# Optimization experiments

Measured on AMD Instinct MI355X. Metric: run time of the kernel, lower is better.

Reference implementation:

```python
import jax, jax.numpy as jnp
import numpy as np

DIM = 512
INNER = 512        # heads(8) * dim_head(64)
OUT_DIM = 256
SCALE = 64 ** -0.5  # dim_head ** -0.5
BN_EPS = 1e-5


def setup_inputs() -> dict:
    key = jax.random.key(0)
    ks = jax.random.split(key, 8)
    B, H, W = 2, 96, 320
    return {
        "left_feat": jax.random.normal(ks[0], (B, DIM, H, W), jnp.float32),
        "right_feat": jax.random.normal(ks[1], (B, DIM, H, W), jnp.float32),
        "wq": jax.random.normal(ks[2], (INNER, DIM), jnp.float32) * (DIM ** -0.5),
        "wk": jax.random.normal(ks[3], (INNER, DIM), jnp.float32) * (DIM ** -0.5),
        "wv": jax.random.normal(ks[4], (INNER, DIM), jnp.float32) * (DIM ** -0.5),
        "w1": jax.random.normal(ks[5], (OUT_DIM, INNER * 2), jnp.float32) * ((INNER * 2) ** -0.5),
        "bn_gamma": jnp.ones((OUT_DIM,), jnp.float32),
        "bn_beta": jnp.zeros((OUT_DIM,), jnp.float32),
        "bn_mean": jnp.zeros((OUT_DIM,), jnp.float32),
        "bn_var": jnp.ones((OUT_DIM,), jnp.float32),
        "w2": jax.random.normal(ks[6], (OUT_DIM, OUT_DIM), jnp.float32) * (OUT_DIM ** -0.5),
    }


def reference(left_feat, right_feat, wq, wk, wv, w1, bn_gamma, bn_beta, bn_mean, bn_var, w2):
    # conv1x1 projections, directly producing channels-last [b, h, w, c]
    q = jnp.einsum('bchw,oc->bhwo', left_feat, wq)
    k = jnp.einsum('bchw,oc->bhwo', right_feat, wk)
    v = jnp.einsum('bchw,oc->bhwo', right_feat, wv)
    # cross-attention along width, independently per (batch, row)
    dots = jnp.einsum('bhwc,bhxc->bhwx', q, k) * SCALE   # [b, h, w, w]
    attn = jax.nn.softmax(dots, axis=-1)
    out = jnp.einsum('bhwx,bhxc->bhwc', attn, v)         # [b, h, w, c]
    out = out.transpose(0, 3, 1, 2)                      # [b, c, h, w]
    new_left = jnp.concatenate([left_feat, out], axis=1)  # [b, 2*inner, h, w]
    # to_out: conv1x1 -> BN (eval mode, running stats) -> LeakyReLU(0.2) -> conv1x1
    y = jnp.einsum('bchw,oc->bohw', new_left, w1)
    inv = jax.lax.rsqrt(bn_var + BN_EPS)
    y = (y - bn_mean[None, :, None, None]) * (inv * bn_gamma)[None, :, None, None] \
        + bn_beta[None, :, None, None]
    y = jnp.where(y >= 0, y, 0.2 * y)
    return jnp.einsum('bchw,oc->bohw', y, w2)
```

## Files before the change

kernel.cpp:

```cpp
#include <hip/hip_runtime.h>

typedef __bf16 bf16x8 __attribute__((ext_vector_type(8)));
typedef float f32x4 __attribute__((ext_vector_type(4)));

#define MFMA16(a, b, c) __builtin_amdgcn_mfma_f32_16x16x32_bf16((a), (b), (c), 0, 0, 0)
#define GLOAD_LDS(gp, lp) __builtin_amdgcn_global_load_lds( \
    (const __attribute__((address_space(1))) void*)(uintptr_t)(const void*)(gp), \
    (__attribute__((address_space(3))) void*)(uintptr_t)(void*)(lp), 16, 0, 0)

#define NB 2
#define NC 512
#define NH 96
#define NW 320
#define PH 30720
#define NPIX 61440
#define NOUT 256

__device__ __forceinline__ unsigned short f2bf(float f) {
    union { float f; unsigned u; } v; v.f = f;
    unsigned r = v.u + 0x7fffu + ((v.u >> 16) & 1u);
    return (unsigned short)(r >> 16);
}

__global__ void k_cast(const float* __restrict__ src, unsigned short* __restrict__ dst, int n) {
    int i = blockIdx.x * 256 + threadIdx.x;
    if (i < n) dst[i] = f2bf(src[i]);
}

__global__ __launch_bounds__(256) void k_transpose(
        const float* __restrict__ L, const float* __restrict__ R,
        unsigned short* __restrict__ Lcl, unsigned short* __restrict__ Rcl) {
    __shared__ float t[64][65];
    int z = blockIdx.z;
    int b = z & 1, which = z >> 1;
    const float* src = which ? R : L;
    unsigned short* dst = which ? Rcl : Lcl;
    int c0 = blockIdx.y * 64;
    int p0 = blockIdx.x * 64;
    int tx = threadIdx.x & 63, ty = threadIdx.x >> 6;
#pragma unroll
    for (int i = 0; i < 16; ++i) {
        int cl = ty + i * 4;
        t[cl][tx] = src[(b * NC + c0 + cl) * PH + p0 + tx];
    }
    __syncthreads();
#pragma unroll
    for (int i = 0; i < 16; ++i) {
        int pl = ty + i * 4;
        dst[(b * PH + p0 + pl) * NC + c0 + tx] = f2bf(t[tx][pl]);
    }
}

template <int MODE>
__global__ __launch_bounds__(256) void k_gemm(
        const unsigned short* __restrict__ A0,
        const unsigned short* __restrict__ A1,
        const unsigned short* __restrict__ Bb,
        unsigned short* __restrict__ Dbf,
        float* __restrict__ Df32,
        const float* __restrict__ g, const float* __restrict__ be,
        const float* __restrict__ mu, const float* __restrict__ va) {
    constexpr int SA = (MODE == 4) ? NOUT : NC;
    constexpr int SB = (MODE == 3) ? 1024 : (MODE == 4) ? NOUT : NC;
    constexpr int KS = (MODE == 3) ? 32 : (MODE == 4) ? 8 : 16;
    constexpr int NTO = (MODE <= 2) ? 4 : 2;
    constexpr int TOT = 480 * NTO;

    __shared__ unsigned short Asm[128 * 32];
    __shared__ unsigned short Bsm[128 * 32];

    int pphys = blockIdx.x;
    int lgc = (pphys & 7) * (TOT / 8) + (pphys >> 3);
    int pixt = lgc / NTO, ot = lgc % NTO;
    const int mbase = ((MODE == 2 || MODE == 4) ? ot : pixt) * 128;
    const int nbase = ((MODE == 2 || MODE == 4) ? pixt : ot) * 128;

    const int lane = threadIdx.x & 63, w = threadIdx.x >> 6;
    const int lr = lane & 15, lg = lane >> 4;
    const int wr = w >> 1, wc = w & 1;

    auto stage = [&](unsigned short* lds, const unsigned short* src, int rowBase, int colOff) {
#pragma unroll
        for (int j = 0; j < 2; ++j) {
            int cb = w * 128 + j * 64;
            int c = cb + lane;
            int rstride = (lds == Asm) ? SA : SB;
            const unsigned short* gp = src + (size_t)(rowBase + (c >> 2)) * rstride + colOff + (c & 3) * 8;
            GLOAD_LDS(gp, lds + cb * 8);
        }
    };

    f32x4 acc[4][4] = {};

    for (int kc = 0; kc < KS; ++kc) {
        if constexpr (MODE == 3) {
            if (kc < 16) stage(Asm, A0, mbase, kc * 32);
            else         stage(Asm, A1, mbase, (kc - 16) * 32);
        } else {
            stage(Asm, A0, mbase, kc * 32);
        }
        stage(Bsm, Bb, nbase, kc * 32);
        __syncthreads();

        bf16x8 af[4], bfr[4];
#pragma unroll
        for (int i = 0; i < 4; ++i)
            af[i] = *reinterpret_cast<const bf16x8*>(Asm + (wr * 64 + i * 16 + lr) * 32 + lg * 8);
#pragma unroll
        for (int j = 0; j < 4; ++j)
            bfr[j] = *reinterpret_cast<const bf16x8*>(Bsm + (wc * 64 + j * 16 + lr) * 32 + lg * 8);
#pragma unroll
        for (int i = 0; i < 4; ++i)
#pragma unroll
            for (int j = 0; j < 4; ++j)
                acc[i][j] = MFMA16(af[i], bfr[j], acc[i][j]);
        __syncthreads();
    }

    const int lr4 = lg * 4;
    if constexpr (MODE <= 1) {
#pragma unroll
        for (int i = 0; i < 4; ++i)
#pragma unroll
            for (int j = 0; j < 4; ++j) {
                int ocol = nbase + wc * 64 + j * 16 + lr;
#pragma unroll
                for (int r = 0; r < 4; ++r) {
                    int prow = mbase + wr * 64 + i * 16 + lr4 + r;
                    Dbf[(size_t)prow * NC + ocol] = f2bf(acc[i][j][r]);
                }
            }
    } else if constexpr (MODE == 2) {
#pragma unroll
        for (int i = 0; i < 4; ++i)
#pragma unroll
            for (int j = 0; j < 4; ++j) {
                int pix = nbase + wc * 64 + j * 16 + lr;
                int b = pix / PH, ph = pix % PH;
                int hh = ph / NW, x = ph % NW;
#pragma unroll
                for (int r = 0; r < 4; ++r) {
                    int crow = mbase + wr * 64 + i * 16 + lr4 + r;
                    Dbf[((size_t)(b * NH + hh) * NC + crow) * NW + x] = f2bf(acc[i][j][r]);
                }
            }
    } else if constexpr (MODE == 3) {
#pragma unroll
        for (int j = 0; j < 4; ++j) {
            int o = nbase + wc * 64 + j * 16 + lr;
            float sc = g[o] * rsqrtf(va[o] + 1e-5f);
            float sh = be[o] - mu[o] * sc;
#pragma unroll
            for (int i = 0; i < 4; ++i)
#pragma unroll
                for (int r = 0; r < 4; ++r) {
                    int prow = mbase + wr * 64 + i * 16 + lr4 + r;
                    float y = acc[i][j][r] * sc + sh;
                    y = (y >= 0.f) ? y : 0.2f * y;
                    Dbf[(size_t)prow * NOUT + o] = f2bf(y);
                }
        }
    } else {
#pragma unroll
        for (int j = 0; j < 4; ++j) {
            int pix = nbase + wc * 64 + j * 16 + lr;
            int b = pix / PH, ph = pix % PH;
#pragma unroll
            for (int i = 0; i < 4; ++i)
#pragma unroll
                for (int r = 0; r < 4; ++r) {
                    int o = mbase + wr * 64 + i * 16 + lr4 + r;
                    Df32[((size_t)b * NOUT + o) * PH + ph] = acc[i][j][r];
                }
        }
    }
}

__global__ __launch_bounds__(256, 2) void k_attn(
        const unsigned short* __restrict__ Q, const unsigned short* __restrict__ K,
        const unsigned short* __restrict__ Vt, unsigned short* __restrict__ O) {
    __shared__ unsigned short P[64][328];
    __shared__ unsigned short KV[32 * 512];

    int pphys = blockIdx.x;
    int l = (pphys & 7) * 120 + (pphys >> 3);
    int head = l / 5, qt = l % 5;
    int b = head / NH, hh = head % NH;
    int lane = threadIdx.x & 63, w = threadIdx.x >> 6;
    int lr = lane & 15, lg = lane >> 4;
    int rowbase = b * PH + hh * NW;
    int qrow = rowbase + qt * 64 + w * 16 + lr;

    bf16x8 qf[16];
#pragma unroll
    for (int kc = 0; kc < 16; ++kc)
        qf[kc] = *reinterpret_cast<const bf16x8*>(Q + (size_t)qrow * NC + kc * 32 + lg * 8);

    f32x4 acc[20];
#pragma unroll
    for (int xt = 0; xt < 20; ++xt) acc[xt] = f32x4{0.f, 0.f, 0.f, 0.f};

#pragma unroll
    for (int s = 0; s < 10; ++s) {
#pragma unroll
        for (int j = 0; j < 8; ++j) {
            int r = w * 8 + j;
            const unsigned short* gp = K + (size_t)(rowbase + s * 32 + r) * NC + ((lane ^ (r & 7)) * 8);
            GLOAD_LDS(gp, KV + r * 512);
        }
        __syncthreads();
#pragma unroll
        for (int x2 = 0; x2 < 2; ++x2) {
            int rrow = x2 * 16 + lr;
            int rsw = lr & 7;
#pragma unroll
            for (int kc = 0; kc < 16; ++kc) {
                bf16x8 kf = *reinterpret_cast<const bf16x8*>(KV + rrow * 512 + (((kc * 4 + lg) ^ rsw) * 8));
                acc[s * 2 + x2] = MFMA16(qf[kc], kf, acc[s * 2 + x2]);
            }
        }
        __syncthreads();
    }

#pragma unroll
    for (int xt = 0; xt < 20; ++xt)
#pragma unroll
        for (int r = 0; r < 4; ++r) acc[xt][r] *= 0.125f;
    float m[4] = {-1e30f, -1e30f, -1e30f, -1e30f};
#pragma unroll
    for (int xt = 0; xt < 20; ++xt)
#pragma unroll
        for (int r = 0; r < 4; ++r) m[r] = fmaxf(m[r], acc[xt][r]);
#pragma unroll
    for (int mask = 1; mask < 16; mask <<= 1)
#pragma unroll
        for (int r = 0; r < 4; ++r) m[r] = fmaxf(m[r], __shfl_xor(m[r], mask));
    float s4[4] = {0.f, 0.f, 0.f, 0.f};
#pragma unroll
    for (int xt = 0; xt < 20; ++xt)
#pragma unroll
        for (int r = 0; r < 4; ++r) {
            float e = __expf(acc[xt][r] - m[r]);
            acc[xt][r] = e;
            s4[r] += e;
        }
#pragma unroll
    for (int mask = 1; mask < 16; mask <<= 1)
#pragma unroll
        for (int r = 0; r < 4; ++r) s4[r] += __shfl_xor(s4[r], mask);
#pragma unroll
    for (int xt = 0; xt < 20; ++xt)
#pragma unroll
        for (int r = 0; r < 4; ++r)
            P[w * 16 + lg * 4 + r][xt * 16 + lr] = f2bf(acc[xt][r]);
    __syncthreads();

    f32x4 oacc[32];
#pragma unroll
    for (int ct = 0; ct < 32; ++ct) oacc[ct] = f32x4{0.f, 0.f, 0.f, 0.f};

    int vbase = (b * NH + hh) * NC;
    for (int s = 0; s < 10; ++s) {
#pragma unroll
        for (int j = 0; j < 8; ++j) {
            int c = (w * 8 + j) * 16 + (lane >> 2);
            int qg = (lane & 3) ^ ((lane >> 3) & 3);
            const unsigned short* gp = Vt + (size_t)(vbase + c) * NW + s * 32 + qg * 8;
            GLOAD_LDS(gp, KV + (w * 8 + j) * 512);
        }
        __syncthreads();
        bf16x8 pf = *reinterpret_cast<const bf16x8*>(&P[w * 16 + lr][s * 32 + lg * 8]);
#pragma unroll
        for (int ct = 0; ct < 32; ++ct) {
            bf16x8 vf = *reinterpret_cast<const bf16x8*>(KV + ct * 512 + lr * 32 + ((lg ^ ((lr >> 1) & 3)) * 8));
            oacc[ct] = MFMA16(pf, vf, oacc[ct]);
        }
        __syncthreads();
    }

#pragma unroll
    for (int ct = 0; ct < 32; ++ct)
#pragma unroll
        for (int r = 0; r < 4; ++r) {
            int prow = rowbase + qt * 64 + w * 16 + lg * 4 + r;
            O[(size_t)prow * NC + ct * 16 + lr] = f2bf(oacc[ct][r] / s4[r]);
        }
}

extern "C" void kernel_launch(void* const* d_in, const int* in_sizes, int n_in,
                              void* d_out, int out_size, void* d_ws, size_t ws_size,
                              hipStream_t stream) {
    const float* left  = (const float*)d_in[0];
    const float* right = (const float*)d_in[1];
    const float* wq = (const float*)d_in[2];
    const float* wk = (const float*)d_in[3];
    const float* wv = (const float*)d_in[4];
    const float* w1 = (const float*)d_in[5];
    const float* bn_g = (const float*)d_in[6];
    const float* bn_b = (const float*)d_in[7];
    const float* bn_m = (const float*)d_in[8];
    const float* bn_v = (const float*)d_in[9];
    const float* w2 = (const float*)d_in[10];
    float* out = (float*)d_out;

    size_t off = 0;
    auto alloc = [&](size_t bytes) -> void* {
        void* p = (char*)d_ws + off;
        off += (bytes + 255) & ~(size_t)255;
        return p;
    };
    const size_t clb = (size_t)NPIX * NC * 2;
    unsigned short* Lcl = (unsigned short*)alloc(clb);
    unsigned short* Rcl = (unsigned short*)alloc(clb);
    unsigned short* Qb  = (unsigned short*)alloc(clb);
    unsigned short* Kb  = (unsigned short*)alloc(clb);
    unsigned short* Vt  = (unsigned short*)alloc(clb);
    unsigned short* Wqb = (unsigned short*)alloc((size_t)NC * NC * 2);
    unsigned short* Wkb = (unsigned short*)alloc((size_t)NC * NC * 2);
    unsigned short* Wvb = (unsigned short*)alloc((size_t)NC * NC * 2);
    unsigned short* W1b = (unsigned short*)alloc((size_t)NOUT * 1024 * 2);
    unsigned short* W2b = (unsigned short*)alloc((size_t)NOUT * NOUT * 2);
    unsigned short* AO = Rcl;
    unsigned short* Yb = Qb;

    k_cast<<<dim3((NC * NC + 255) / 256), 256, 0, stream>>>(wq, Wqb, NC * NC);
    k_cast<<<dim3((NC * NC + 255) / 256), 256, 0, stream>>>(wk, Wkb, NC * NC);
    k_cast<<<dim3((NC * NC + 255) / 256), 256, 0, stream>>>(wv, Wvb, NC * NC);
    k_cast<<<dim3((NOUT * 1024 + 255) / 256), 256, 0, stream>>>(w1, W1b, NOUT * 1024);
    k_cast<<<dim3((NOUT * NOUT + 255) / 256), 256, 0, stream>>>(w2, W2b, NOUT * NOUT);

    k_transpose<<<dim3(PH / 64, NC / 64, 4), 256, 0, stream>>>(left, right, Lcl, Rcl);

    k_gemm<0><<<dim3(1920), 256, 0, stream>>>(Lcl, nullptr, Wqb, Qb, nullptr, nullptr, nullptr, nullptr, nullptr);
    k_gemm<1><<<dim3(1920), 256, 0, stream>>>(Rcl, nullptr, Wkb, Kb, nullptr, nullptr, nullptr, nullptr, nullptr);
    k_gemm<2><<<dim3(1920), 256, 0, stream>>>(Wvb, nullptr, Rcl, Vt, nullptr, nullptr, nullptr, nullptr, nullptr);

    k_attn<<<dim3(960), 256, 0, stream>>>(Qb, Kb, Vt, AO);

    k_gemm<3><<<dim3(960), 256, 0, stream>>>(Lcl, AO, W1b, Yb, nullptr, bn_g, bn_b, bn_m, bn_v);

    k_gemm<4><<<dim3(960), 256, 0, stream>>>(W2b, nullptr, Yb, nullptr, out, nullptr, nullptr, nullptr, nullptr);
}
```

Measured before the change: 429.4 us.

## Fuse K/V projections into one kernel and register-prefetch K/V tiles in attention

Replaces the separate K and V projection GEMMs with a single kernel that loads each right-feature tile once and computes both K and the transposed V, so the shared input is read from memory only once. In the attention kernel, the direct global-to-LDS loads are replaced by register prefetch of the next K or V tile into a double-buffered LDS region, with setprio around the MFMA blocks, so loads can overlap compute. The cost is more registers and an extra barrier per step, which may lower occupancy.

```diff
diff --git a/kernel.cpp b/kernel.cpp
--- a/kernel.cpp
+++ b/kernel.cpp
@@ -2,6 +2,7 @@
 
 typedef __bf16 bf16x8 __attribute__((ext_vector_type(8)));
 typedef float f32x4 __attribute__((ext_vector_type(4)));
+typedef unsigned short u16x8 __attribute__((ext_vector_type(8)));
 
 #define MFMA16(a, b, c) __builtin_amdgcn_mfma_f32_16x16x32_bf16((a), (b), (c), 0, 0, 0)
 #define GLOAD_LDS(gp, lp) __builtin_amdgcn_global_load_lds( \
@@ -130,20 +131,6 @@
                     Dbf[(size_t)prow * NC + ocol] = f2bf(acc[i][j][r]);
                 }
             }
-    } else if constexpr (MODE == 2) {
-#pragma unroll
-        for (int i = 0; i < 4; ++i)
-#pragma unroll
-            for (int j = 0; j < 4; ++j) {
-                int pix = nbase + wc * 64 + j * 16 + lr;
-                int b = pix / PH, ph = pix % PH;
-                int hh = ph / NW, x = ph % NW;
-#pragma unroll
-                for (int r = 0; r < 4; ++r) {
-                    int crow = mbase + wr * 64 + i * 16 + lr4 + r;
-                    Dbf[((size_t)(b * NH + hh) * NC + crow) * NW + x] = f2bf(acc[i][j][r]);
-                }
-            }
     } else if constexpr (MODE == 3) {
 #pragma unroll
         for (int j = 0; j < 4; ++j) {
@@ -174,6 +161,93 @@
                 }
         }
     }
+}
+
+__global__ __launch_bounds__(256) void k_projkv(
+        const unsigned short* __restrict__ Rcl,
+        const unsigned short* __restrict__ Wk, const unsigned short* __restrict__ Wv,
+        unsigned short* __restrict__ Kb, unsigned short* __restrict__ Vt) {
+    __shared__ unsigned short Rsm[128 * 32];
+    __shared__ unsigned short Ksm[128 * 32];
+    __shared__ unsigned short Vsm[128 * 32];
+
+    int pphys = blockIdx.x;
+    int lgc = (pphys & 7) * 240 + (pphys >> 3);
+    int pixt = lgc / 4, j4 = lgc % 4;
+    const int pbase = pixt * 128;
+    const int obase = j4 * 128;
+
+    const int lane = threadIdx.x & 63, w = threadIdx.x >> 6;
+    const int lr = lane & 15, lg = lane >> 4;
+    const int wr = w >> 1, wc = w & 1;
+
+    auto stage = [&](unsigned short* lds, const unsigned short* src, int rowBase, int colOff) {
+#pragma unroll
+        for (int j = 0; j < 2; ++j) {
+            int cb = w * 128 + j * 64;
+            int c = cb + lane;
+            const unsigned short* gp = src + (size_t)(rowBase + (c >> 2)) * NC + colOff + (c & 3) * 8;
+            GLOAD_LDS(gp, lds + cb * 8);
+        }
+    };
+
+    f32x4 ak[4][4] = {};
+    f32x4 av[4][4] = {};
+
+    for (int kc = 0; kc < 16; ++kc) {
+        stage(Rsm, Rcl, pbase, kc * 32);
+        stage(Ksm, Wk, obase, kc * 32);
+        stage(Vsm, Wv, obase, kc * 32);
+        __syncthreads();
+
+        bf16x8 ra[4], rb[4], kb[4], va[4];
+#pragma unroll
+        for (int i = 0; i < 4; ++i) {
+            ra[i] = *reinterpret_cast<const bf16x8*>(Rsm + (wr * 64 + i * 16 + lr) * 32 + lg * 8);
+            va[i] = *reinterpret_cast<const bf16x8*>(Vsm + (wr * 64 + i * 16 + lr) * 32 + lg * 8);
+        }
+#pragma unroll
+        for (int j = 0; j < 4; ++j) {
+            rb[j] = *reinterpret_cast<const bf16x8*>(Rsm + (wc * 64 + j * 16 + lr) * 32 + lg * 8);
+            kb[j] = *reinterpret_cast<const bf16x8*>(Ksm + (wc * 64 + j * 16 + lr) * 32 + lg * 8);
+        }
+        __builtin_amdgcn_s_setprio(1);
+#pragma unroll
+        for (int i = 0; i < 4; ++i)
+#pragma unroll
+            for (int j = 0; j < 4; ++j) {
+                ak[i][j] = MFMA16(ra[i], kb[j], ak[i][j]);
+                av[i][j] = MFMA16(va[i], rb[j], av[i][j]);
+            }
+        __builtin_amdgcn_s_setprio(0);
+        __syncthreads();
+    }
+
+    const int lr4 = lg * 4;
+#pragma unroll
+    for (int i = 0; i < 4; ++i)
+#pragma unroll
+        for (int j = 0; j < 4; ++j) {
+            int ocol = obase + wc * 64 + j * 16 + lr;
+#pragma unroll
+            for (int r = 0; r < 4; ++r) {
+                int prow = pbase + wr * 64 + i * 16 + lr4 + r;
+                Kb[(size_t)prow * NC + ocol] = f2bf(ak[i][j][r]);
+            }
+        }
+#pragma unroll
+    for (int i = 0; i < 4; ++i)
+#pragma unroll
+        for (int j = 0; j < 4; ++j) {
+            int pix = pbase + wc * 64 + j * 16 + lr;
+            int b = pix / PH, ph = pix % PH;
+            int hh = ph / NW, x = ph % NW;
+#pragma unroll
+            for (int r = 0; r < 4; ++r) {
+                int crow = obase + wr * 64 + i * 16 + lr4 + r;
+                Vt[((size_t)(b * NH + hh) * NC + crow) * NW + x] = f2bf(av[i][j][r]);
+            }
+        }
 }
 
 __global__ __launch_bounds__(256, 2) void k_attn(
@@ -200,27 +274,61 @@
 #pragma unroll
     for (int xt = 0; xt < 20; ++xt) acc[xt] = f32x4{0.f, 0.f, 0.f, 0.f};
 
-#pragma unroll
-    for (int s = 0; s < 10; ++s) {
+    u16x8 kreg[4];
+    auto kload = [&](int t) {
+#pragma unroll
+        for (int j = 0; j < 4; ++j) {
+            int r = w * 4 + j;
+            kreg[j] = *reinterpret_cast<const u16x8*>(
+                K + (size_t)(rowbase + t * 16 + r) * NC + ((lane ^ (r & 7)) * 8));
+        }
+    };
+    auto kwrite = [&](int buf) {
+#pragma unroll
+        for (int j = 0; j < 4; ++j) {
+            int r = w * 4 + j;
+            *reinterpret_cast<u16x8*>(KV + (buf * 16 + r) * 512 + lane * 8) = kreg[j];
+        }
+    };
+
+    kload(0);
+    kwrite(0);
+    __syncthreads();
+#pragma unroll
+    for (int t = 0; t < 20; ++t) {
+        if (t + 1 < 20) kload(t + 1);
+        int buf = t & 1;
+        int rsw = lr & 7;
+        __builtin_amdgcn_s_setprio(1);
+#pragma unroll
+        for (int kc = 0; kc < 16; ++kc) {
+            bf16x8 kf = *reinterpret_cast<const bf16x8*>(
+                KV + (buf * 16 + lr) * 512 + (((kc * 4 + lg) ^ rsw) * 8));
+            acc[t] = MFMA16(qf[kc], kf, acc[t]);
+        }
+        __builtin_amdgcn_s_setprio(0);
+        __syncthreads();
+        if (t + 1 < 20) kwrite(buf ^ 1);
+        __syncthreads();
+    }
+
+    int vbase = (b * NH + hh) * NC;
+    u16x8 vreg[8];
+    auto vload = [&](int s) {
 #pragma unroll
         for (int j = 0; j < 8; ++j) {
-            int r = w * 8 + j;
-            const unsigned short* gp = K + (size_t)(rowbase + s * 32 + r) * NC + ((lane ^ (r & 7)) * 8);
-            GLOAD_LDS(gp, KV + r * 512);
-        }
-        __syncthreads();
-#pragma unroll
-        for (int x2 = 0; x2 < 2; ++x2) {
-            int rrow = x2 * 16 + lr;
-            int rsw = lr & 7;
-#pragma unroll
-            for (int kc = 0; kc < 16; ++kc) {
-                bf16x8 kf = *reinterpret_cast<const bf16x8*>(KV + rrow * 512 + (((kc * 4 + lg) ^ rsw) * 8));
-                acc[s * 2 + x2] = MFMA16(qf[kc], kf, acc[s * 2 + x2]);
-            }
-        }
-        __syncthreads();
-    }
+            int c = (w * 8 + j) * 16 + (lane >> 2);
+            int qg = (lane & 3) ^ ((lane >> 3) & 3);
+            vreg[j] = *reinterpret_cast<const u16x8*>(
+                Vt + (size_t)(vbase + c) * NW + s * 32 + qg * 8);
+        }
+    };
+    auto vwrite = [&]() {
+#pragma unroll
+        for (int j = 0; j < 8; ++j)
+            *reinterpret_cast<u16x8*>(KV + (w * 8 + j) * 512 + lane * 8) = vreg[j];
+    };
+    vload(0);
 
 #pragma unroll
     for (int xt = 0; xt < 20; ++xt)
@@ -254,27 +362,27 @@
         for (int r = 0; r < 4; ++r)
             P[w * 16 + lg * 4 + r][xt * 16 + lr] = f2bf(acc[xt][r]);
     __syncthreads();
+    vwrite();
+    __syncthreads();
 
     f32x4 oacc[32];
 #pragma unroll
     for (int ct = 0; ct < 32; ++ct) oacc[ct] = f32x4{0.f, 0.f, 0.f, 0.f};
 
-    int vbase = (b * NH + hh) * NC;
+#pragma unroll
     for (int s = 0; s < 10; ++s) {
-#pragma unroll
-        for (int j = 0; j < 8; ++j) {
-            int c = (w * 8 + j) * 16 + (lane >> 2);
-            int qg = (lane & 3) ^ ((lane >> 3) & 3);
-            const unsigned short* gp = Vt + (size_t)(vbase + c) * NW + s * 32 + qg * 8;
-            GLOAD_LDS(gp, KV + (w * 8 + j) * 512);
-        }
-        __syncthreads();
+        if (s + 1 < 10) vload(s + 1);
         bf16x8 pf = *reinterpret_cast<const bf16x8*>(&P[w * 16 + lr][s * 32 + lg * 8]);
+        __builtin_amdgcn_s_setprio(1);
 #pragma unroll
         for (int ct = 0; ct < 32; ++ct) {
-            bf16x8 vf = *reinterpret_cast<const bf16x8*>(KV + ct * 512 + lr * 32 + ((lg ^ ((lr >> 1) & 3)) * 8));
+            bf16x8 vf = *reinterpret_cast<const bf16x8*>(
+                KV + ct * 512 + lr * 32 + ((lg ^ ((lr >> 1) & 3)) * 8));
             oacc[ct] = MFMA16(pf, vf, oacc[ct]);
         }
+        __builtin_amdgcn_s_setprio(0);
+        __syncthreads();
+        if (s + 1 < 10) vwrite();
         __syncthreads();
     }
 
@@ -332,8 +440,7 @@
     k_transpose<<<dim3(PH / 64, NC / 64, 4), 256, 0, stream>>>(left, right, Lcl, Rcl);
 
     k_gemm<0><<<dim3(1920), 256, 0, stream>>>(Lcl, nullptr, Wqb, Qb, nullptr, nullptr, nullptr, nullptr, nullptr);
-    k_gemm<1><<<dim3(1920), 256, 0, stream>>>(Rcl, nullptr, Wkb, Kb, nullptr, nullptr, nullptr, nullptr, nullptr);
-    k_gemm<2><<<dim3(1920), 256, 0, stream>>>(Wvb, nullptr, Rcl, Vt, nullptr, nullptr, nullptr, nullptr, nullptr);
+    k_projkv<<<dim3(1920), 256, 0, stream>>>(Rcl, Wkb, Wvb, Kb, Vt);
 
     k_attn<<<dim3(960), 256, 0, stream>>>(Qb, Kb, Vt, AO);
 
```

Result: slower. 507.2 us (+18.1%).

## Double-buffer GEMM LDS tiles and prefetch attention K/V through registers

Applied to the files above, without the earlier changes.

The GEMM kernel now uses two LDS buffers per operand, so the next K-slice is issued before the MFMAs on the current one, with one barrier per iteration instead of two. The attention kernel replaces the direct global-to-LDS K and V loads with register prefetch: the next tile is loaded into registers while MFMAs run on the current LDS tile, then written to LDS. The K tile shrinks to 16 rows in a double buffer, and the first V tile is prefetched during the softmax. s_setprio raises wave priority around the MFMA blocks. The changes aim to hide global-load latency, but they double GEMM LDS use and add register pressure in the already register-heavy attention kernel, which could lower occupancy.

```diff
diff --git a/kernel.cpp b/kernel.cpp
--- a/kernel.cpp
+++ b/kernel.cpp
@@ -2,6 +2,7 @@
 
 typedef __bf16 bf16x8 __attribute__((ext_vector_type(8)));
 typedef float f32x4 __attribute__((ext_vector_type(4)));
+typedef unsigned short u16x8 __attribute__((ext_vector_type(8)));
 
 #define MFMA16(a, b, c) __builtin_amdgcn_mfma_f32_16x16x32_bf16((a), (b), (c), 0, 0, 0)
 #define GLOAD_LDS(gp, lp) __builtin_amdgcn_global_load_lds( \
@@ -66,8 +67,8 @@
     constexpr int NTO = (MODE <= 2) ? 4 : 2;
     constexpr int TOT = 480 * NTO;
 
-    __shared__ unsigned short Asm[128 * 32];
-    __shared__ unsigned short Bsm[128 * 32];
+    __shared__ unsigned short Asm[2][128 * 32];
+    __shared__ unsigned short Bsm[2][128 * 32];
 
     int pphys = blockIdx.x;
     int lgc = (pphys & 7) * (TOT / 8) + (pphys >> 3);
@@ -79,41 +80,56 @@
     const int lr = lane & 15, lg = lane >> 4;
     const int wr = w >> 1, wc = w & 1;
 
-    auto stage = [&](unsigned short* lds, const unsigned short* src, int rowBase, int colOff) {
+    auto stageA = [&](int buf, int kc) {
+        const unsigned short* srcA = A0;
+        int colOff = kc * 32;
+        if constexpr (MODE == 3) {
+            if (kc >= 16) { srcA = A1; colOff = (kc - 16) * 32; }
+        }
 #pragma unroll
         for (int j = 0; j < 2; ++j) {
             int cb = w * 128 + j * 64;
             int c = cb + lane;
-            int rstride = (lds == Asm) ? SA : SB;
-            const unsigned short* gp = src + (size_t)(rowBase + (c >> 2)) * rstride + colOff + (c & 3) * 8;
-            GLOAD_LDS(gp, lds + cb * 8);
+            const unsigned short* gp = srcA + (size_t)(mbase + (c >> 2)) * SA + colOff + (c & 3) * 8;
+            GLOAD_LDS(gp, Asm[buf] + cb * 8);
+        }
+    };
+    auto stageB = [&](int buf, int kc) {
+#pragma unroll
+        for (int j = 0; j < 2; ++j) {
+            int cb = w * 128 + j * 64;
+            int c = cb + lane;
+            const unsigned short* gp = Bb + (size_t)(nbase + (c >> 2)) * SB + kc * 32 + (c & 3) * 8;
+            GLOAD_LDS(gp, Bsm[buf] + cb * 8);
         }
     };
 
     f32x4 acc[4][4] = {};
 
+    stageA(0, 0);
+    stageB(0, 0);
+    __syncthreads();
+
     for (int kc = 0; kc < KS; ++kc) {
-        if constexpr (MODE == 3) {
-            if (kc < 16) stage(Asm, A0, mbase, kc * 32);
-            else         stage(Asm, A1, mbase, (kc - 16) * 32);
-        } else {
-            stage(Asm, A0, mbase, kc * 32);
-        }
-        stage(Bsm, Bb, nbase, kc * 32);
-        __syncthreads();
-
+        int cur = kc & 1;
+        if (kc + 1 < KS) {
+            stageA(cur ^ 1, kc + 1);
+            stageB(cur ^ 1, kc + 1);
+        }
         bf16x8 af[4], bfr[4];
 #pragma unroll
         for (int i = 0; i < 4; ++i)
-            af[i] = *reinterpret_cast<const bf16x8*>(Asm + (wr * 64 + i * 16 + lr) * 32 + lg * 8);
+            af[i] = *reinterpret_cast<const bf16x8*>(Asm[cur] + (wr * 64 + i * 16 + lr) * 32 + lg * 8);
 #pragma unroll
         for (int j = 0; j < 4; ++j)
-            bfr[j] = *reinterpret_cast<const bf16x8*>(Bsm + (wc * 64 + j * 16 + lr) * 32 + lg * 8);
+            bfr[j] = *reinterpret_cast<const bf16x8*>(Bsm[cur] + (wc * 64 + j * 16 + lr) * 32 + lg * 8);
+        __builtin_amdgcn_s_setprio(1);
 #pragma unroll
         for (int i = 0; i < 4; ++i)
 #pragma unroll
             for (int j = 0; j < 4; ++j)
                 acc[i][j] = MFMA16(af[i], bfr[j], acc[i][j]);
+        __builtin_amdgcn_s_setprio(0);
         __syncthreads();
     }
 
@@ -200,27 +216,61 @@
 #pragma unroll
     for (int xt = 0; xt < 20; ++xt) acc[xt] = f32x4{0.f, 0.f, 0.f, 0.f};
 
-#pragma unroll
-    for (int s = 0; s < 10; ++s) {
+    u16x8 kreg[4];
+    auto kload = [&](int t) {
+#pragma unroll
+        for (int j = 0; j < 4; ++j) {
+            int r = w * 4 + j;
+            kreg[j] = *reinterpret_cast<const u16x8*>(
+                K + (size_t)(rowbase + t * 16 + r) * NC + ((lane ^ (r & 7)) * 8));
+        }
+    };
+    auto kwrite = [&](int buf) {
+#pragma unroll
+        for (int j = 0; j < 4; ++j) {
+            int r = w * 4 + j;
+            *reinterpret_cast<u16x8*>(KV + (buf * 16 + r) * 512 + lane * 8) = kreg[j];
+        }
+    };
+
+    kload(0);
+    kwrite(0);
+    __syncthreads();
+#pragma unroll
+    for (int t = 0; t < 20; ++t) {
+        if (t + 1 < 20) kload(t + 1);
+        int buf = t & 1;
+        int rsw = lr & 7;
+        __builtin_amdgcn_s_setprio(1);
+#pragma unroll
+        for (int kc = 0; kc < 16; ++kc) {
+            bf16x8 kf = *reinterpret_cast<const bf16x8*>(
+                KV + (buf * 16 + lr) * 512 + (((kc * 4 + lg) ^ rsw) * 8));
+            acc[t] = MFMA16(qf[kc], kf, acc[t]);
+        }
+        __builtin_amdgcn_s_setprio(0);
+        __syncthreads();
+        if (t + 1 < 20) kwrite(buf ^ 1);
+        __syncthreads();
+    }
+
+    int vbase = (b * NH + hh) * NC;
+    u16x8 vreg[8];
+    auto vload = [&](int s) {
 #pragma unroll
         for (int j = 0; j < 8; ++j) {
-            int r = w * 8 + j;
-            const unsigned short* gp = K + (size_t)(rowbase + s * 32 + r) * NC + ((lane ^ (r & 7)) * 8);
-            GLOAD_LDS(gp, KV + r * 512);
-        }
-        __syncthreads();
-#pragma unroll
-        for (int x2 = 0; x2 < 2; ++x2) {
-            int rrow = x2 * 16 + lr;
-            int rsw = lr & 7;
-#pragma unroll
-            for (int kc = 0; kc < 16; ++kc) {
-                bf16x8 kf = *reinterpret_cast<const bf16x8*>(KV + rrow * 512 + (((kc * 4 + lg) ^ rsw) * 8));
-                acc[s * 2 + x2] = MFMA16(qf[kc], kf, acc[s * 2 + x2]);
-            }
-        }
-        __syncthreads();
-    }
+            int c = (w * 8 + j) * 16 + (lane >> 2);
+            int qg = (lane & 3) ^ ((lane >> 3) & 3);
+            vreg[j] = *reinterpret_cast<const u16x8*>(
+                Vt + (size_t)(vbase + c) * NW + s * 32 + qg * 8);
+        }
+    };
+    auto vwrite = [&]() {
+#pragma unroll
+        for (int j = 0; j < 8; ++j)
+            *reinterpret_cast<u16x8*>(KV + (w * 8 + j) * 512 + lane * 8) = vreg[j];
+    };
+    vload(0);
 
 #pragma unroll
     for (int xt = 0; xt < 20; ++xt)
@@ -254,27 +304,27 @@
         for (int r = 0; r < 4; ++r)
             P[w * 16 + lg * 4 + r][xt * 16 + lr] = f2bf(acc[xt][r]);
     __syncthreads();
+    vwrite();
+    __syncthreads();
 
     f32x4 oacc[32];
 #pragma unroll
     for (int ct = 0; ct < 32; ++ct) oacc[ct] = f32x4{0.f, 0.f, 0.f, 0.f};
 
-    int vbase = (b * NH + hh) * NC;
+#pragma unroll
     for (int s = 0; s < 10; ++s) {
-#pragma unroll
-        for (int j = 0; j < 8; ++j) {
-            int c = (w * 8 + j) * 16 + (lane >> 2);
-            int qg = (lane & 3) ^ ((lane >> 3) & 3);
-            const unsigned short* gp = Vt + (size_t)(vbase + c) * NW + s * 32 + qg * 8;
-            GLOAD_LDS(gp, KV + (w * 8 + j) * 512);
-        }
-        __syncthreads();
+        if (s + 1 < 10) vload(s + 1);
         bf16x8 pf = *reinterpret_cast<const bf16x8*>(&P[w * 16 + lr][s * 32 + lg * 8]);
+        __builtin_amdgcn_s_setprio(1);
 #pragma unroll
         for (int ct = 0; ct < 32; ++ct) {
-            bf16x8 vf = *reinterpret_cast<const bf16x8*>(KV + ct * 512 + lr * 32 + ((lg ^ ((lr >> 1) & 3)) * 8));
+            bf16x8 vf = *reinterpret_cast<const bf16x8*>(
+                KV + ct * 512 + lr * 32 + ((lg ^ ((lr >> 1) & 3)) * 8));
             oacc[ct] = MFMA16(pf, vf, oacc[ct]);
         }
+        __builtin_amdgcn_s_setprio(0);
+        __syncthreads();
+        if (s + 1 < 10) vwrite();
         __syncthreads();
     }
 
```

Result: faster. 407.3 us (-5.2%).
